# Kernel optimization log

Measured on AMD Instinct MI355X. Metric: run time of the kernel, lower is better.

## Reference

```python
import jax, jax.numpy as jnp
import numpy as np

DV = 128
DE = 128
EPS = 1e-5

def _gelu(x):
    return jax.nn.gelu(x, approximate=False)  # torch nn.GELU default = erf

def _ln(x, g, b):
    m = jnp.mean(x, axis=-1, keepdims=True)
    v = jnp.mean(jnp.square(x - m), axis=-1, keepdims=True)
    return (x - m) / jnp.sqrt(v + EPS) * g + b

def _mlp3(x, w1, b1, w2, b2, w3, b3):  # d_in->h (act) -> h->h (act) -> h->out
    h = _gelu(x @ w1 + b1)
    h = _gelu(h @ w2 + b2)
    return h @ w3 + b3

def _mlp2(x, w1, b1, w2, b2):  # d_in->h (act) -> h->out
    return _gelu(x @ w1 + b1) @ w2 + b2

def _gather_nodes(V, K):
    # V: [Z,N,Dv], K: [Z,N,Kn] -> Vj[z,n,k] = V[z, K[z,n,k]]
    Vj = jax.vmap(lambda v, k: v[k])(V, K)  # [Z,N,Kn,Dv]
    Vi = jnp.broadcast_to(V[:, :, None, :], Vj.shape)
    return Vi, Vj

def setup_inputs() -> dict:
    key = jax.random.key(0)
    ks = jax.random.split(key, 24)
    Z, N, Kn = 4, 1024, 48
    d_msg_in = 2 * DV + DE  # 384
    p = lambda k, shp: (0.02 * jax.random.normal(k, shp, dtype=jnp.float32))
    inp = {
        'V': jax.random.normal(ks[0], (Z, N, DV), dtype=jnp.float32),
        'E': jax.random.normal(ks[1], (Z, N, Kn, DE), dtype=jnp.float32),
        'edge_mask': jnp.ones((Z, N, Kn), dtype=jnp.float32),
        # node messenger MLP (hidden_layers=1): 384->128, 128->128, 128->128
        'nm_w1': p(ks[2], (d_msg_in, DV)), 'nm_b1': jnp.zeros((DV,), jnp.float32),
        'nm_w2': p(ks[3], (DV, DV)), 'nm_b2': jnp.zeros((DV,), jnp.float32),
        'nm_w3': p(ks[4], (DV, DV)), 'nm_b3': jnp.zeros((DV,), jnp.float32),
        'nmn_g': jnp.ones((DV,), jnp.float32), 'nmn_b': jnp.zeros((DV,), jnp.float32),
        # ffn (hidden_layers=0): 128->512, 512->128
        'ffn_w1': p(ks[5], (DV, 4 * DV)), 'ffn_b1': jnp.zeros((4 * DV,), jnp.float32),
        'ffn_w2': p(ks[6], (4 * DV, DV)), 'ffn_b2': jnp.zeros((DV,), jnp.float32),
        'fn_g': jnp.ones((DV,), jnp.float32), 'fn_b': jnp.zeros((DV,), jnp.float32),
        # edge messenger MLP (hidden_layers=1): 384->128, 128->128, 128->128
        'em_w1': p(ks[7], (d_msg_in, DE)), 'em_b1': jnp.zeros((DE,), jnp.float32),
        'em_w2': p(ks[8], (DE, DE)), 'em_b2': jnp.zeros((DE,), jnp.float32),
        'em_w3': p(ks[9], (DE, DE)), 'em_b3': jnp.zeros((DE,), jnp.float32),
        'emn_g': jnp.ones((DE,), jnp.float32), 'emn_b': jnp.zeros((DE,), jnp.float32),
        'K': jax.random.randint(ks[10], (Z, N, Kn), 0, N, dtype=jnp.int64),
    }
    return inp

def reference(V, E, edge_mask,
              nm_w1, nm_b1, nm_w2, nm_b2, nm_w3, nm_b3, nmn_g, nmn_b,
              ffn_w1, ffn_b1, ffn_w2, ffn_b2, fn_g, fn_b,
              em_w1, em_b1, em_w2, em_b2, em_w3, em_b3, emn_g, emn_b,
              K):
    m = edge_mask[..., None]  # [Z,N,Kn,1]
    # node message pass
    Vi, Vj = _gather_nodes(V, K)
    Mv_pre = jnp.concatenate([Vi, Vj, E], axis=3)  # [Z,N,Kn,2Dv+De]
    Mv = _mlp3(Mv_pre, nm_w1, nm_b1, nm_w2, nm_b2, nm_w3, nm_b3) * m
    V = _ln(V + jnp.sum(Mv, axis=2), nmn_g, nmn_b)
    # ffn
    V = _ln(V + _mlp2(V, ffn_w1, ffn_b1, ffn_w2, ffn_b2), fn_g, fn_b)
    # edge message pass
    Vi, Vj = _gather_nodes(V, K)
    Me_pre = jnp.concatenate([Vi, Vj, E], axis=3)
    Me = _mlp3(Me_pre, em_w1, em_b1, em_w2, em_b2, em_w3, em_b3) * m
    E = _ln(E + Me, emn_g, emn_b)
    return (V, E)
```

## Files before the change

### kernel.cpp

```cpp
#include <hip/hip_runtime.h>
#include <hip/hip_bf16.h>

using bf16 = __hip_bfloat16;
typedef __attribute__((ext_vector_type(8))) short short8;
typedef __attribute__((ext_vector_type(4))) float f32x4;

#define ZN 4096
#define KN 48

__device__ __forceinline__ float gelu_f(float x) {
    return 0.5f * x * (1.0f + erff(x * 0.70710678118654752440f));
}

__device__ __forceinline__ uint2 pack4(float a, float b, float c, float d) {
    union { bf16 h[4]; uint2 u; } t;
    t.h[0] = __float2bfloat16(a); t.h[1] = __float2bfloat16(b);
    t.h[2] = __float2bfloat16(c); t.h[3] = __float2bfloat16(d);
    return t.u;
}

__global__ void pack_all_kernel(const float* __restrict__ nm1, const float* __restrict__ nm2,
                                const float* __restrict__ nm3, const float* __restrict__ em1,
                                const float* __restrict__ em2, const float* __restrict__ em3,
                                bf16* __restrict__ P) {
    int idx = blockIdx.x * 256 + threadIdx.x;
    const float* W; int local;
    if      (idx <  49152) { W = nm1; local = idx;          }
    else if (idx <  65536) { W = nm2; local = idx -  49152; }
    else if (idx <  81920) { W = nm3; local = idx -  65536; }
    else if (idx < 131072) { W = em1; local = idx -  81920; }
    else if (idx < 147456) { W = em2; local = idx - 131072; }
    else                   { W = em3; local = idx - 147456; }
    int j    = local & 7;
    int lane = (local >> 3) & 63;
    int nt   = (local >> 9) & 7;
    int ks   = local >> 12;
    int k = ks * 32 + ((lane >> 4) << 3) + j;
    int n = nt * 16 + (lane & 15);
    P[idx] = __float2bfloat16(W[k * 128 + n]);
}

__global__ void pack_ffn_kernel(const float* __restrict__ w1, const float* __restrict__ w2,
                                bf16* __restrict__ P1, bf16* __restrict__ P2) {
    int idx = blockIdx.x * 256 + threadIdx.x;
    if (idx < 65536) {
        int local = idx;
        int j = local & 7, lane = (local >> 3) & 63, nt = (local >> 9) & 31, ks = local >> 14;
        int k = ks * 32 + ((lane >> 4) << 3) + j;
        int n = nt * 16 + (lane & 15);
        P1[local] = __float2bfloat16(w1[k * 512 + n]);
    } else {
        int local = idx - 65536;
        int j = local & 7, lane = (local >> 3) & 63, nt = (local >> 9) & 7, ks = local >> 12;
        int k = ks * 32 + ((lane >> 4) << 3) + j;
        int n = nt * 16 + (lane & 15);
        P2[local] = __float2bfloat16(w2[k * 128 + n]);
    }
}

template<int KSBEG, int NSTEPS>
__device__ __forceinline__ void do_gemm(const bf16* A, int ldA, const bf16* Bp,
                                        int lane, int nt0, f32x4 acc[3][2]) {
    #pragma unroll
    for (int s = 0; s < NSTEPS; ++s) {
        int ks = KSBEG + s;
        short8 b0 = *(const short8*)(Bp + (((ks * 8 + nt0) * 64 + lane) << 3));
        short8 b1 = *(const short8*)(Bp + (((ks * 8 + nt0 + 1) * 64 + lane) << 3));
        int kcol = s * 32 + ((lane >> 4) << 3);
        #pragma unroll
        for (int mt = 0; mt < 3; ++mt) {
            short8 a = *(const short8*)(A + (mt * 16 + (lane & 15)) * ldA + kcol);
            acc[mt][0] = __builtin_amdgcn_mfma_f32_16x16x32_bf16(a, b0, acc[mt][0], 0, 0, 0);
            acc[mt][1] = __builtin_amdgcn_mfma_f32_16x16x32_bf16(a, b1, acc[mt][1], 0, 0, 0);
        }
    }
}

template<int NSTEPS, int NT, int NACC>
__device__ __forceinline__ void do_gemm_1m(const bf16* A, int ldA, const bf16* Bp,
                                           int lane, int nt0, f32x4 acc[NACC]) {
    #pragma unroll
    for (int s = 0; s < NSTEPS; ++s) {
        int kcol = s * 32 + ((lane >> 4) << 3);
        short8 a = *(const short8*)(A + (lane & 15) * ldA + kcol);
        #pragma unroll
        for (int ni = 0; ni < NACC; ++ni) {
            short8 b = *(const short8*)(Bp + (((s * NT + nt0 + ni) * 64 + lane) << 3));
            acc[ni] = __builtin_amdgcn_mfma_f32_16x16x32_bf16(a, b, acc[ni], 0, 0, 0);
        }
    }
}

__global__ __launch_bounds__(256, 4)
void yvi_mfma_kernel(const float* __restrict__ Vsrc, const bf16* __restrict__ w1p,
                     const float* __restrict__ b1f, bf16* __restrict__ out)
{
    __shared__ __align__(16) bf16 sA[16][136];
    const int nb  = blockIdx.x * 16;
    const int tid = threadIdx.x;
    const int lane = tid & 63, wid = tid >> 6;
    for (int c = tid; c < 16 * 32; c += 256) {
        int r = c >> 5, off = (c & 31) * 4;
        float4 v = *(const float4*)(Vsrc + (size_t)(nb + r) * 128 + off);
        *(uint2*)&sA[r][off] = pack4(v.x, v.y, v.z, v.w);
    }
    __syncthreads();
    const int nt0 = wid * 2;
    f32x4 acc[2];
    acc[0] = (f32x4){0.f,0.f,0.f,0.f}; acc[1] = (f32x4){0.f,0.f,0.f,0.f};
    do_gemm_1m<4, 8, 2>(&sA[0][0], 136, w1p, lane, nt0, acc);
    const int lm = lane & 15, lg = lane >> 4;
    #pragma unroll
    for (int ni = 0; ni < 2; ++ni) {
        int col = (nt0 + ni) * 16 + lm;
        float bv = b1f[col];
        #pragma unroll
        for (int r = 0; r < 4; ++r)
            out[(size_t)(nb + lg * 4 + r) * 128 + col] = __float2bfloat16(acc[ni][r] + bv);
    }
}

__global__ __launch_bounds__(256, 2)
void ffn_mfma_kernel(const bf16* __restrict__ V1,
                     const bf16* __restrict__ w1p, const float* __restrict__ b1,
                     const bf16* __restrict__ w2p, const float* __restrict__ b2,
                     const float* __restrict__ g, const float* __restrict__ bta,
                     float* __restrict__ Vout)
{
    __shared__ __align__(16) bf16 sA[16][136];
    __shared__ __align__(16) bf16 sH[16][520];
    __shared__ float sX[16][132];
    const int nb  = blockIdx.x * 16;
    const int tid = threadIdx.x;
    const int lane = tid & 63, wid = tid >> 6;
    const int lm = lane & 15, lg = lane >> 4;
    {
        int c = tid;
        int r = c >> 4, off = (c & 15) * 8;
        *(uint4*)&sA[r][off] = *(const uint4*)(V1 + (size_t)(nb + r) * 128 + off);
    }
    __syncthreads();
    {
        f32x4 acc[8];
        #pragma unroll
        for (int i = 0; i < 8; ++i) acc[i] = (f32x4){0.f,0.f,0.f,0.f};
        do_gemm_1m<4, 32, 8>(&sA[0][0], 136, w1p, lane, wid * 8, acc);
        #pragma unroll
        for (int ni = 0; ni < 8; ++ni) {
            int col = (wid * 8 + ni) * 16 + lm;
            float bv = b1[col];
            #pragma unroll
            for (int r = 0; r < 4; ++r)
                sH[lg * 4 + r][col] = __float2bfloat16(gelu_f(acc[ni][r] + bv));
        }
    }
    __syncthreads();
    {
        f32x4 acc[2];
        acc[0] = (f32x4){0.f,0.f,0.f,0.f}; acc[1] = (f32x4){0.f,0.f,0.f,0.f};
        do_gemm_1m<16, 8, 2>(&sH[0][0], 520, w2p, lane, wid * 2, acc);
        #pragma unroll
        for (int ni = 0; ni < 2; ++ni) {
            int col = (wid * 2 + ni) * 16 + lm;
            float bv = b2[col];
            #pragma unroll
            for (int r = 0; r < 4; ++r) {
                int row = lg * 4 + r;
                sX[row][col] = __bfloat162float(sA[row][col]) + acc[ni][r] + bv;
            }
        }
    }
    __syncthreads();
    for (int n = wid; n < 16; n += 4) {
        float a = sX[n][lane], b = sX[n][lane + 64];
        float s = a + b, q = a * a + b * b;
        #pragma unroll
        for (int off = 32; off; off >>= 1) { s += __shfl_xor(s, off); q += __shfl_xor(q, off); }
        float mean = s * (1.f / 128.f);
        float var  = q * (1.f / 128.f) - mean * mean;
        float rs   = rsqrtf(var + 1e-5f);
        size_t base = (size_t)(nb + n) * 128;
        Vout[base + lane]      = (a - mean) * rs * g[lane]      + bta[lane];
        Vout[base + lane + 64] = (b - mean) * rs * g[lane + 64] + bta[lane + 64];
    }
}

__global__ __launch_bounds__(256, 5)
void msg_node_kernel(const float* __restrict__ Vf,
                     const float* __restrict__ Ef,
                     const float* __restrict__ maskf,
                     const int*   __restrict__ Kidx,
                     const bf16*  __restrict__ Yvi,
                     const bf16* __restrict__ w1p,
                     const bf16* __restrict__ w2p, const float* __restrict__ b2f,
                     const bf16* __restrict__ w3p, const float* __restrict__ b3f,
                     const float* __restrict__ lng, const float* __restrict__ lnb,
                     const float* __restrict__ Vres,
                     bf16*  __restrict__ V1out)
{
    __shared__ __align__(16) char region0[26112];
    __shared__ float sYvi[128];
    __shared__ float sMask[48];
    __shared__ float sS[128];

    bf16  (*sA)[264]  = reinterpret_cast<bf16(*)[264]>(region0);
    bf16  (*sH1)[136] = reinterpret_cast<bf16(*)[136]>(region0);
    bf16  (*sH2)[136] = reinterpret_cast<bf16(*)[136]>(region0 + 13056);

    const int node = blockIdx.x;
    const int tid  = threadIdx.x;
    const int lane = tid & 63;
    const int wid  = tid >> 6;
    const int z    = node >> 10;
    const int* krow = Kidx + node * KN;

    if (tid < 128) sYvi[tid] = __bfloat162float(Yvi[(size_t)node * 128 + tid]);
    if (tid >= 128 && tid < 128 + KN)
        sMask[tid - 128] = maskf[(size_t)node * KN + (tid - 128)];
    {
        const float* erow0 = Ef + (size_t)node * KN * 128;
        for (int c = tid; c < KN * 32; c += 256) {
            int r = c >> 5;
            int off = (c & 31) * 4;
            int kj = krow[r];
            float4 vj = *(const float4*)(Vf + ((size_t)(z * 1024 + kj)) * 128 + off);
            *(uint2*)&sA[r][off] = pack4(vj.x, vj.y, vj.z, vj.w);
            float4 ee = *(const float4*)(erow0 + r * 128 + off);
            *(uint2*)&sA[r][128 + off] = pack4(ee.x, ee.y, ee.z, ee.w);
        }
    }
    __syncthreads();

    const int nt0 = wid * 2;
    const int lm  = lane & 15;
    const int lg  = lane >> 4;
    const f32x4 vzero = {0.f, 0.f, 0.f, 0.f};

    f32x4 acc[3][2];
    #pragma unroll
    for (int mt = 0; mt < 3; ++mt) { acc[mt][0] = vzero; acc[mt][1] = vzero; }
    do_gemm<4, 8>(&sA[0][0], 264, w1p, lane, nt0, acc);
    __syncthreads();
    #pragma unroll
    for (int mt = 0; mt < 3; ++mt)
    #pragma unroll
    for (int ni = 0; ni < 2; ++ni) {
        int col = (nt0 + ni) * 16 + lm;
        float yv = sYvi[col];
        #pragma unroll
        for (int r = 0; r < 4; ++r) {
            int row = mt * 16 + lg * 4 + r;
            sH1[row][col] = __float2bfloat16(gelu_f(acc[mt][ni][r] + yv));
        }
    }
    __syncthreads();

    #pragma unroll
    for (int mt = 0; mt < 3; ++mt) { acc[mt][0] = vzero; acc[mt][1] = vzero; }
    do_gemm<0, 4>(&sH1[0][0], 136, w2p, lane, nt0, acc);
    {
        float bc0 = b2f[nt0 * 16 + lm];
        float bc1 = b2f[(nt0 + 1) * 16 + lm];
        #pragma unroll
        for (int mt = 0; mt < 3; ++mt)
        #pragma unroll
        for (int r = 0; r < 4; ++r) {
            int row = mt * 16 + lg * 4 + r;
            sH2[row][nt0 * 16 + lm]       = __float2bfloat16(gelu_f(acc[mt][0][r] + bc0));
            sH2[row][(nt0 + 1) * 16 + lm] = __float2bfloat16(gelu_f(acc[mt][1][r] + bc1));
        }
    }
    __syncthreads();

    #pragma unroll
    for (int mt = 0; mt < 3; ++mt) { acc[mt][0] = vzero; acc[mt][1] = vzero; }
    do_gemm<0, 4>(&sH2[0][0], 136, w3p, lane, nt0, acc);
    {
        float bc0 = b3f[nt0 * 16 + lm];
        float bc1 = b3f[(nt0 + 1) * 16 + lm];
        float cs0 = 0.f, cs1 = 0.f;
        #pragma unroll
        for (int mt = 0; mt < 3; ++mt)
        #pragma unroll
        for (int r = 0; r < 4; ++r) {
            float m = sMask[mt * 16 + lg * 4 + r];
            cs0 += (acc[mt][0][r] + bc0) * m;
            cs1 += (acc[mt][1][r] + bc1) * m;
        }
        cs0 += __shfl_xor(cs0, 16); cs0 += __shfl_xor(cs0, 32);
        cs1 += __shfl_xor(cs1, 16); cs1 += __shfl_xor(cs1, 32);
        if (lane < 16) {
            sS[nt0 * 16 + lane]       = cs0;
            sS[(nt0 + 1) * 16 + lane] = cs1;
        }
    }
    __syncthreads();

    if (tid < 64) {
        float a = Vres[(size_t)node * 128 + tid]      + sS[tid];
        float b = Vres[(size_t)node * 128 + tid + 64] + sS[tid + 64];
        float s = a + b, q = a * a + b * b;
        #pragma unroll
        for (int off = 32; off; off >>= 1) { s += __shfl_xor(s, off); q += __shfl_xor(q, off); }
        float mean = s * (1.f / 128.f);
        float var  = q * (1.f / 128.f) - mean * mean;
        float rs   = rsqrtf(var + 1e-5f);
        V1out[(size_t)node * 128 + tid] =
            __float2bfloat16((a - mean) * rs * lng[tid] + lnb[tid]);
        V1out[(size_t)node * 128 + tid + 64] =
            __float2bfloat16((b - mean) * rs * lng[tid + 64] + lnb[tid + 64]);
    }
}

__global__ __launch_bounds__(256, 5)
void mlp_edge_kernel(const float* __restrict__ Vf,
                     const float* __restrict__ Ef,
                     const float* __restrict__ maskf,
                     const int*   __restrict__ Kidx,
                     const bf16*  __restrict__ Yvi,
                     const bf16* __restrict__ w1p,
                     const bf16* __restrict__ w2p, const float* __restrict__ b2f,
                     const bf16* __restrict__ w3p, const float* __restrict__ b3f,
                     float* __restrict__ MeOut)
{
    __shared__ __align__(16) char region0[26112];
    __shared__ float sYvi[128];
    __shared__ float sMask[48];

    bf16  (*sA)[264]  = reinterpret_cast<bf16(*)[264]>(region0);
    bf16  (*sH1)[136] = reinterpret_cast<bf16(*)[136]>(region0);
    bf16  (*sH2)[136] = reinterpret_cast<bf16(*)[136]>(region0 + 13056);

    const int node = blockIdx.x;
    const int tid  = threadIdx.x;
    const int lane = tid & 63;
    const int wid  = tid >> 6;
    const int z    = node >> 10;
    const int* krow = Kidx + node * KN;

    if (tid < 128) sYvi[tid] = __bfloat162float(Yvi[(size_t)node * 128 + tid]);
    if (tid >= 128 && tid < 128 + KN)
        sMask[tid - 128] = maskf[(size_t)node * KN + (tid - 128)];
    {
        const float* erow0 = Ef + (size_t)node * KN * 128;
        for (int c = tid; c < KN * 32; c += 256) {
            int r = c >> 5;
            int off = (c & 31) * 4;
            int kj = krow[r];
            float4 vj = *(const float4*)(Vf + ((size_t)(z * 1024 + kj)) * 128 + off);
            *(uint2*)&sA[r][off] = pack4(vj.x, vj.y, vj.z, vj.w);
            float4 ee = *(const float4*)(erow0 + r * 128 + off);
            *(uint2*)&sA[r][128 + off] = pack4(ee.x, ee.y, ee.z, ee.w);
        }
    }
    __syncthreads();

    const int nt0 = wid * 2;
    const int lm  = lane & 15;
    const int lg  = lane >> 4;
    const f32x4 vzero = {0.f, 0.f, 0.f, 0.f};

    f32x4 acc[3][2];
    #pragma unroll
    for (int mt = 0; mt < 3; ++mt) { acc[mt][0] = vzero; acc[mt][1] = vzero; }
    do_gemm<4, 8>(&sA[0][0], 264, w1p, lane, nt0, acc);
    __syncthreads();
    #pragma unroll
    for (int mt = 0; mt < 3; ++mt)
    #pragma unroll
    for (int ni = 0; ni < 2; ++ni) {
        int col = (nt0 + ni) * 16 + lm;
        float yv = sYvi[col];
        #pragma unroll
        for (int r = 0; r < 4; ++r) {
            int row = mt * 16 + lg * 4 + r;
            sH1[row][col] = __float2bfloat16(gelu_f(acc[mt][ni][r] + yv));
        }
    }
    __syncthreads();

    #pragma unroll
    for (int mt = 0; mt < 3; ++mt) { acc[mt][0] = vzero; acc[mt][1] = vzero; }
    do_gemm<0, 4>(&sH1[0][0], 136, w2p, lane, nt0, acc);
    {
        float bc0 = b2f[nt0 * 16 + lm];
        float bc1 = b2f[(nt0 + 1) * 16 + lm];
        #pragma unroll
        for (int mt = 0; mt < 3; ++mt)
        #pragma unroll
        for (int r = 0; r < 4; ++r) {
            int row = mt * 16 + lg * 4 + r;
            sH2[row][nt0 * 16 + lm]       = __float2bfloat16(gelu_f(acc[mt][0][r] + bc0));
            sH2[row][(nt0 + 1) * 16 + lm] = __float2bfloat16(gelu_f(acc[mt][1][r] + bc1));
        }
    }
    __syncthreads();

    #pragma unroll
    for (int mt = 0; mt < 3; ++mt) { acc[mt][0] = vzero; acc[mt][1] = vzero; }
    do_gemm<0, 4>(&sH2[0][0], 136, w3p, lane, nt0, acc);
    {
        float bc0 = b3f[nt0 * 16 + lm];
        float bc1 = b3f[(nt0 + 1) * 16 + lm];
        float* meRow = MeOut + (size_t)node * KN * 128;
        #pragma unroll
        for (int mt = 0; mt < 3; ++mt)
        #pragma unroll
        for (int r = 0; r < 4; ++r) {
            int row = mt * 16 + lg * 4 + r;
            float m = sMask[row];
            meRow[row * 128 + nt0 * 16 + lm]       = (acc[mt][0][r] + bc0) * m;
            meRow[row * 128 + (nt0 + 1) * 16 + lm] = (acc[mt][1][r] + bc1) * m;
        }
    }
}

__global__ __launch_bounds__(256, 8)
void ln_edge_kernel(const float* __restrict__ Ef,
                    float* __restrict__ Me,
                    const float* __restrict__ g, const float* __restrict__ b)
{
    const int row  = blockIdx.x * 4 + (threadIdx.x >> 6);
    const int lane = threadIdx.x & 63;
    const size_t base = (size_t)row * 128;
    float2 me = ((const float2*)(Me + base))[lane];
    float2 ev = ((const float2*)(Ef + base))[lane];
    float x0 = ev.x + me.x;
    float x1 = ev.y + me.y;
    float s = x0 + x1, q = x0 * x0 + x1 * x1;
    #pragma unroll
    for (int off = 32; off; off >>= 1) { s += __shfl_xor(s, off); q += __shfl_xor(q, off); }
    float mean = s * (1.f / 128.f);
    float var  = q * (1.f / 128.f) - mean * mean;
    float rs   = rsqrtf(var + 1e-5f);
    float2 o;
    o.x = (x0 - mean) * rs * g[2 * lane]     + b[2 * lane];
    o.y = (x1 - mean) * rs * g[2 * lane + 1] + b[2 * lane + 1];
    ((float2*)(Me + base))[lane] = o;
}

extern "C" void kernel_launch(void* const* d_in, const int* in_sizes, int n_in,
                              void* d_out, int out_size, void* d_ws, size_t ws_size,
                              hipStream_t stream) {
    const float* V     = (const float*)d_in[0];
    const float* E     = (const float*)d_in[1];
    const float* emask = (const float*)d_in[2];
    const float* nm_w1 = (const float*)d_in[3];
    const float* nm_b1 = (const float*)d_in[4];
    const float* nm_w2 = (const float*)d_in[5];
    const float* nm_b2 = (const float*)d_in[6];
    const float* nm_w3 = (const float*)d_in[7];
    const float* nm_b3 = (const float*)d_in[8];
    const float* nmn_g = (const float*)d_in[9];
    const float* nmn_b = (const float*)d_in[10];
    const float* ffn_w1 = (const float*)d_in[11];
    const float* ffn_b1 = (const float*)d_in[12];
    const float* ffn_w2 = (const float*)d_in[13];
    const float* ffn_b2 = (const float*)d_in[14];
    const float* fn_g  = (const float*)d_in[15];
    const float* fn_b  = (const float*)d_in[16];
    const float* em_w1 = (const float*)d_in[17];
    const float* em_b1 = (const float*)d_in[18];
    const float* em_w2 = (const float*)d_in[19];
    const float* em_b2 = (const float*)d_in[20];
    const float* em_w3 = (const float*)d_in[21];
    const float* em_b3 = (const float*)d_in[22];
    const float* emn_g = (const float*)d_in[23];
    const float* emn_b = (const float*)d_in[24];
    const int*  K     = (const int*)d_in[25];

    char* ws = (char*)d_ws;
    bf16* Pall    = (bf16*)(ws);
    bf16* p_nm_w1 = (bf16*)(ws);
    bf16* p_nm_w2 = (bf16*)(ws + 98304);
    bf16* p_nm_w3 = (bf16*)(ws + 131072);
    bf16* p_em_w1 = (bf16*)(ws + 163840);
    bf16* p_em_w2 = (bf16*)(ws + 262144);
    bf16* p_em_w3 = (bf16*)(ws + 294912);
    bf16* V1f  = (bf16*)(ws + 327680);
    bf16* YviE = (bf16*)(ws + 327680);
    bf16* YviN = (bf16*)(ws + 327680 + 1048576);

    float* V2out = (float*)d_out;
    float* Eout  = (float*)d_out + 524288;

    bf16* fw1p = (bf16*)((float*)d_out + 25690112 - 65536);
    bf16* fw2p = (bf16*)((float*)d_out + 25690112 - 32768);

    pack_all_kernel<<<640, 256, 0, stream>>>(nm_w1, nm_w2, nm_w3, em_w1, em_w2, em_w3, Pall);
    pack_ffn_kernel<<<512, 256, 0, stream>>>(ffn_w1, ffn_w2, fw1p, fw2p);

    yvi_mfma_kernel<<<ZN / 16, 256, 0, stream>>>(V, p_nm_w1, nm_b1, YviN);

    msg_node_kernel<<<ZN, 256, 0, stream>>>(
        V, E, emask, K, YviN,
        p_nm_w1, p_nm_w2, nm_b2, p_nm_w3, nm_b3,
        nmn_g, nmn_b, V, V1f);

    ffn_mfma_kernel<<<ZN / 16, 256, 0, stream>>>(
        V1f, fw1p, ffn_b1, fw2p, ffn_b2, fn_g, fn_b, V2out);

    yvi_mfma_kernel<<<ZN / 16, 256, 0, stream>>>(V2out, p_em_w1, em_b1, YviE);

    mlp_edge_kernel<<<ZN, 256, 0, stream>>>(
        V2out, E, emask, K, YviE,
        p_em_w1, p_em_w2, em_b2, p_em_w3, em_b3,
        Eout);

    ln_edge_kernel<<<ZN * KN / 4, 256, 0, stream>>>(E, Eout, emn_g, emn_b);
}
```

Measured before the change: 192.4 us.

## Fuse edge residual-add and LayerNorm into edge MLP kernel epilogue

Removes the separate edge LayerNorm kernel. The edge MLP kernel now adds E to the masked message and computes per-row statistics with shuffles plus a small shared-memory cross-wave reduction, then writes the normalized output directly. This avoids writing the intermediate message to global memory and reading it back along with E in another launch. In exchange it adds registers for the held values, an extra barrier, and re-reads E from global memory in the epilogue.

```diff
diff --git a/kernel.cpp b/kernel.cpp
--- a/kernel.cpp
+++ b/kernel.cpp
@@ -321,11 +321,13 @@
                      const bf16* __restrict__ w1p,
                      const bf16* __restrict__ w2p, const float* __restrict__ b2f,
                      const bf16* __restrict__ w3p, const float* __restrict__ b3f,
-                     float* __restrict__ MeOut)
+                     const float* __restrict__ lng, const float* __restrict__ lnb,
+                     float* __restrict__ Eout)
 {
     __shared__ __align__(16) char region0[26112];
     __shared__ float sYvi[128];
     __shared__ float sMask[48];
+    __shared__ float sPart[48][4][2];
 
     bf16  (*sA)[264]  = reinterpret_cast<bf16(*)[264]>(region0);
     bf16  (*sH1)[136] = reinterpret_cast<bf16(*)[136]>(region0);
@@ -399,44 +401,49 @@
     #pragma unroll
     for (int mt = 0; mt < 3; ++mt) { acc[mt][0] = vzero; acc[mt][1] = vzero; }
     do_gemm<0, 4>(&sH2[0][0], 136, w3p, lane, nt0, acc);
+
+    float xv[3][4][2];
     {
         float bc0 = b3f[nt0 * 16 + lm];
         float bc1 = b3f[(nt0 + 1) * 16 + lm];
-        float* meRow = MeOut + (size_t)node * KN * 128;
+        const float* erow0 = Ef + (size_t)node * KN * 128;
         #pragma unroll
         for (int mt = 0; mt < 3; ++mt)
         #pragma unroll
         for (int r = 0; r < 4; ++r) {
             int row = mt * 16 + lg * 4 + r;
             float m = sMask[row];
-            meRow[row * 128 + nt0 * 16 + lm]       = (acc[mt][0][r] + bc0) * m;
-            meRow[row * 128 + (nt0 + 1) * 16 + lm] = (acc[mt][1][r] + bc1) * m;
-        }
-    }
-}
-
-__global__ __launch_bounds__(256, 8)
-void ln_edge_kernel(const float* __restrict__ Ef,
-                    float* __restrict__ Me,
-                    const float* __restrict__ g, const float* __restrict__ b)
-{
-    const int row  = blockIdx.x * 4 + (threadIdx.x >> 6);
-    const int lane = threadIdx.x & 63;
-    const size_t base = (size_t)row * 128;
-    float2 me = ((const float2*)(Me + base))[lane];
-    float2 ev = ((const float2*)(Ef + base))[lane];
-    float x0 = ev.x + me.x;
-    float x1 = ev.y + me.y;
-    float s = x0 + x1, q = x0 * x0 + x1 * x1;
-    #pragma unroll
-    for (int off = 32; off; off >>= 1) { s += __shfl_xor(s, off); q += __shfl_xor(q, off); }
-    float mean = s * (1.f / 128.f);
-    float var  = q * (1.f / 128.f) - mean * mean;
-    float rs   = rsqrtf(var + 1e-5f);
-    float2 o;
-    o.x = (x0 - mean) * rs * g[2 * lane]     + b[2 * lane];
-    o.y = (x1 - mean) * rs * g[2 * lane + 1] + b[2 * lane + 1];
-    ((float2*)(Me + base))[lane] = o;
+            float x0 = erow0[row * 128 + nt0 * 16 + lm]       + (acc[mt][0][r] + bc0) * m;
+            float x1 = erow0[row * 128 + (nt0 + 1) * 16 + lm] + (acc[mt][1][r] + bc1) * m;
+            xv[mt][r][0] = x0; xv[mt][r][1] = x1;
+            float s = x0 + x1, q = x0 * x0 + x1 * x1;
+            s += __shfl_xor(s, 1); q += __shfl_xor(q, 1);
+            s += __shfl_xor(s, 2); q += __shfl_xor(q, 2);
+            s += __shfl_xor(s, 4); q += __shfl_xor(q, 4);
+            s += __shfl_xor(s, 8); q += __shfl_xor(q, 8);
+            if (lm == 0) { sPart[row][wid][0] = s; sPart[row][wid][1] = q; }
+        }
+    }
+    __syncthreads();
+
+    {
+        float g0 = lng[nt0 * 16 + lm],       b0 = lnb[nt0 * 16 + lm];
+        float g1 = lng[(nt0 + 1) * 16 + lm], b1 = lnb[(nt0 + 1) * 16 + lm];
+        float* orow0 = Eout + (size_t)node * KN * 128;
+        #pragma unroll
+        for (int mt = 0; mt < 3; ++mt)
+        #pragma unroll
+        for (int r = 0; r < 4; ++r) {
+            int row = mt * 16 + lg * 4 + r;
+            float s = sPart[row][0][0] + sPart[row][1][0] + sPart[row][2][0] + sPart[row][3][0];
+            float q = sPart[row][0][1] + sPart[row][1][1] + sPart[row][2][1] + sPart[row][3][1];
+            float mean = s * (1.f / 128.f);
+            float var  = q * (1.f / 128.f) - mean * mean;
+            float rs   = rsqrtf(var + 1e-5f);
+            orow0[row * 128 + nt0 * 16 + lm]       = (xv[mt][r][0] - mean) * rs * g0 + b0;
+            orow0[row * 128 + (nt0 + 1) * 16 + lm] = (xv[mt][r][1] - mean) * rs * g1 + b1;
+        }
+    }
 }
 
 extern "C" void kernel_launch(void* const* d_in, const int* in_sizes, int n_in,
@@ -505,7 +512,5 @@
     mlp_edge_kernel<<<ZN, 256, 0, stream>>>(
         V2out, E, emask, K, YviE,
         p_em_w1, p_em_w2, em_b2, p_em_w3, em_b3,
-        Eout);
-
-    ln_edge_kernel<<<ZN * KN / 4, 256, 0, stream>>>(E, Eout, emn_g, emn_b);
-}
+        emn_g, emn_b, Eout);
+}
```

New measurement: 171.6 us. -10.8%, faster.
